# Optimization experiments

Hardware: AMD Instinct MI355X
Metric: run time of the kernel (lower is better)

Reference implementation:

```python
import jax, jax.numpy as jnp
import numpy as np

DK, DV, DMODEL, HEADNUM = 64, 64, 1024, 16
SEQ = 4096


def setup_inputs() -> dict:
    key = jax.random.key(0)
    ks = jax.random.split(key, 7)
    s = 0.02
    return {
        "q": jax.random.normal(ks[0], (SEQ, DMODEL), dtype=jnp.float32),
        "k": jax.random.normal(ks[1], (SEQ, DMODEL), dtype=jnp.float32),
        "v": jax.random.normal(ks[2], (SEQ, DMODEL), dtype=jnp.float32),
        # per-head projection weights, stored batched: [H, dmodel, dk]
        "Wq": jax.random.normal(ks[3], (HEADNUM, DMODEL, DK), dtype=jnp.float32) * s,
        "Wk": jax.random.normal(ks[4], (HEADNUM, DMODEL, DK), dtype=jnp.float32) * s,
        "Wv": jax.random.normal(ks[5], (HEADNUM, DMODEL, DV), dtype=jnp.float32) * s,
        # output linear (torch Linear weight [out, in]; y = x @ W.T)
        "Wo": jax.random.normal(ks[6], (DK * HEADNUM, DK * HEADNUM), dtype=jnp.float32) * s,
    }


def reference(q, k, v, Wq, Wk, Wv, Wo):
    # batched per-head projections: [H, S, dk/dv]
    qh = jnp.einsum("sd,hdk->hsk", q, Wq)
    kh = jnp.einsum("sd,hdk->hsk", k, Wk)
    vh = jnp.einsum("sd,hdv->hsv", v, Wv)
    scale = 1.0 / jnp.sqrt(jnp.asarray(DK, dtype=qh.dtype))
    scores = jnp.einsum("hqk,hsk->hqs", qh, kh) * scale  # [H, S, S]
    attn = jax.nn.softmax(scores, axis=-1)
    heads = jnp.einsum("hqs,hsv->hqv", attn, vh)  # [H, S, dv]
    # concat heads along feature dim: [S, H*dv]
    head_cat = jnp.transpose(heads, (1, 0, 2)).reshape(SEQ, HEADNUM * DV)
    return head_cat @ Wo.T
```

## Files before the change

### kernel.cpp

```cpp
#include <hip/hip_runtime.h>

#define SEQ 4096
#define DMODEL 1024
#define HEADNUM 16
#define DHEAD 64

typedef __attribute__((ext_vector_type(8))) short short8;
typedef __attribute__((ext_vector_type(4))) float f32x4;
typedef __attribute__((ext_vector_type(2))) float f32x2;
typedef __attribute__((ext_vector_type(16))) float f32x16;
typedef __attribute__((ext_vector_type(4))) int i32x4;

__device__ __forceinline__ short f2bf(float f) {
    unsigned u = __float_as_uint(f);
    u = (u + 0x7fffu + ((u >> 16) & 1u)) >> 16;
    return (short)u;
}

__device__ __forceinline__ float bf2f(short s) {
    return __uint_as_float(((unsigned)(unsigned short)s) << 16);
}

__device__ __forceinline__ short8 cvt8(const float4 a, const float4 b) {
    short8 r;
    r[0] = f2bf(a.x); r[1] = f2bf(a.y); r[2] = f2bf(a.z); r[3] = f2bf(a.w);
    r[4] = f2bf(b.x); r[5] = f2bf(b.y); r[6] = f2bf(b.z); r[7] = f2bf(b.w);
    return r;
}

__device__ __forceinline__ int cvtpk_bf16(float lo, float hi) {
    int r;
    asm("v_cvt_pk_bf16_f32 %0, %1, %2" : "=v"(r) : "v"(lo), "v"(hi));
    return r;
}

__device__ __forceinline__ float fexp2(float x) {
    float r;
    asm("v_exp_f32 %0, %1" : "=v"(r) : "v"(x));
    return r;
}

__device__ __forceinline__ void perml32(int& a, int& b) {
    asm("v_permlane32_swap_b32 %0, %1" : "+v"(a), "+v"(b));
}

__device__ __forceinline__ void gld16(const void* g, void* l) {
    __builtin_amdgcn_global_load_lds(
        (const __attribute__((address_space(1))) void*)g,
        (__attribute__((address_space(3))) void*)l, 16, 0, 0);
}

__global__ __launch_bounds__(256) void wtrans_kernel(
    const float* __restrict__ Wq, const float* __restrict__ Wk,
    const float* __restrict__ Wv, short* __restrict__ WT) {
    int which = blockIdx.z;
    const float* W = which == 0 ? Wq : (which == 1 ? Wk : Wv);
    short* dst = WT + (size_t)which * (HEADNUM * DHEAD * DMODEL);
    int h = blockIdx.y, d0 = blockIdx.x * 64;
    int tid = threadIdx.x;
    int c = tid & 63, r4 = tid >> 6;
    __shared__ short tl[64][66];
#pragma unroll
    for (int i = 0; i < 16; ++i) {
        int d = i * 4 + r4;
        tl[c][d] = f2bf(W[((size_t)h * DMODEL + d0 + d) * DHEAD + c]);
    }
    __syncthreads();
#pragma unroll
    for (int i = 0; i < 16; ++i) {
        int n = i * 4 + r4;
        dst[((size_t)h * DHEAD + n) * DMODEL + d0 + c] = tl[n][c];
    }
}

__global__ __launch_bounds__(256) void cast3_kernel(
    const float* __restrict__ q, const float* __restrict__ k,
    const float* __restrict__ v, short* __restrict__ qb,
    short* __restrict__ kb, short* __restrict__ vb) {
    int i = blockIdx.x * 256 + threadIdx.x;
    int seg = i >> 19;
    int off = i & ((1 << 19) - 1);
    const float* src = seg == 0 ? q : (seg == 1 ? k : v);
    short* dst = seg == 0 ? qb : (seg == 1 ? kb : vb);
    const float4* p = (const float4*)(src + (size_t)off * 8);
    *(short8*)(dst + (size_t)off * 8) = cvt8(p[0], p[1]);
}

__global__ __launch_bounds__(256) void cast_bf16_kernel(const float* __restrict__ in,
                                                        short* __restrict__ out, int n8) {
    int i = blockIdx.x * 256 + threadIdx.x;
    if (i >= n8) return;
    const float4* p = (const float4*)(in + (size_t)i * 8);
    *(short8*)(out + (size_t)i * 8) = cvt8(p[0], p[1]);
}

__global__ __launch_bounds__(256) void gemm_kernel(
    const short* __restrict__ A, const short* __restrict__ Bw,
    short* __restrict__ outb, float* __restrict__ outf, int mode) {
    int b = blockIdx.x;
    int wgid = (b & 7) * 64 + (b >> 3);
    int bi = wgid >> 3;
    int ni = wgid & 7;
    int i0 = bi * 64, j0 = ni * 128;

    int tid = threadIdx.x;
    int lane = tid & 63;
    int wv = tid >> 6;
    int l15 = lane & 15;
    int g = lane >> 4;
    int wm = wv >> 1, wn = wv & 1;

    __shared__ char glds[2][24576];

    int ja0 = tid * 16, ja1 = ja0 + 4096;
    int sa0 = (ja0 >> 7) * 2048 + ((ja0 & 127) ^ (((ja0 >> 7) & 7) << 4));
    int sa1 = (ja1 >> 7) * 2048 + ((ja1 & 127) ^ (((ja1 >> 7) & 7) << 4));
    int jb0 = tid * 16, jb1 = jb0 + 4096, jb2 = jb0 + 8192, jb3 = jb0 + 12288;
    int sb0 = (jb0 >> 7) * 2048 + ((jb0 & 127) ^ (((jb0 >> 7) & 7) << 4));
    int sb1 = (jb1 >> 7) * 2048 + ((jb1 & 127) ^ (((jb1 >> 7) & 7) << 4));
    int sb2 = (jb2 >> 7) * 2048 + ((jb2 & 127) ^ (((jb2 >> 7) & 7) << 4));
    int sb3 = (jb3 >> 7) * 2048 + ((jb3 & 127) ^ (((jb3 >> 7) & 7) << 4));

    const char* Ab = (const char*)A + (size_t)i0 * 2048;
    const char* Bb = (const char*)Bw + (size_t)j0 * 2048;

#define GSTAGE(bi_, kt_)                        \
    {                                           \
        char* la_ = glds[bi_];                  \
        char* lb_ = glds[bi_] + 8192;           \
        const char* As = Ab + (kt_) * 128;      \
        const char* Bs = Bb + (kt_) * 128;      \
        gld16(As + sa0, la_ + ja0);             \
        gld16(As + sa1, la_ + ja1);             \
        gld16(Bs + sb0, lb_ + jb0);             \
        gld16(Bs + sb1, lb_ + jb1);             \
        gld16(Bs + sb2, lb_ + jb2);             \
        gld16(Bs + sb3, lb_ + jb3);             \
    }

    f32x4 acc[2][4];
#pragma unroll
    for (int mm = 0; mm < 2; ++mm)
#pragma unroll
        for (int nn = 0; nn < 4; ++nn) acc[mm][nn] = (f32x4){0.f, 0.f, 0.f, 0.f};

    GSTAGE(0, 0);
    int cur = 0;
    for (int kt = 0; kt < 16; ++kt) {
        __syncthreads();
        if (kt < 15) GSTAGE(cur ^ 1, kt + 1);
        const char* la = glds[cur];
        const char* lb = glds[cur] + 8192;
#pragma unroll
        for (int kc = 0; kc < 2; ++kc) {
            short8 af[2], bf4[4];
#pragma unroll
            for (int mm = 0; mm < 2; ++mm) {
                int ra = wm * 32 + mm * 16 + l15;
                af[mm] = *(const short8*)(la + ra * 128 + ((kc * 64 + g * 16) ^ ((ra & 7) << 4)));
            }
#pragma unroll
            for (int nn = 0; nn < 4; ++nn) {
                int rb = wn * 64 + nn * 16 + l15;
                bf4[nn] = *(const short8*)(lb + rb * 128 + ((kc * 64 + g * 16) ^ ((rb & 7) << 4)));
            }
#pragma unroll
            for (int mm = 0; mm < 2; ++mm)
#pragma unroll
                for (int nn = 0; nn < 4; ++nn)
                    acc[mm][nn] = __builtin_amdgcn_mfma_f32_16x16x32_bf16(af[mm], bf4[nn], acc[mm][nn], 0, 0, 0);
        }
        cur ^= 1;
    }
#undef GSTAGE

#pragma unroll
    for (int mm = 0; mm < 2; ++mm)
#pragma unroll
        for (int nn = 0; nn < 4; ++nn)
#pragma unroll
            for (int r = 0; r < 4; ++r) {
                int mg = i0 + wm * 32 + mm * 16 + 4 * g + r;
                int ng = j0 + wn * 64 + nn * 16 + l15;
                float val = acc[mm][nn][r];
                if (mode == 0)      outb[(size_t)mg * 1024 + ng] = f2bf(val);
                else if (mode == 1) outb[(size_t)ng * 4096 + mg] = f2bf(val);
                else                outf[(size_t)mg * 1024 + ng] = val;
            }
}

__global__ __launch_bounds__(256, 4) void attn_kernel(
    const short* __restrict__ qh, const short* __restrict__ kh,
    const short* __restrict__ vt, short* __restrict__ po, float* __restrict__ ml) {
    int b = blockIdx.x;
    int wg = ((b & 7) << 7) | (b >> 3);
    int h = wg >> 6;
    int rem = wg & 63;
    int half = rem >> 5;
    int qb = rem & 31;

    int tid = threadIdx.x;
    int lane = tid & 63;
    int wv = tid >> 6;
    int l31 = lane & 31;
    int hh = lane >> 5;
    int qbase = qb * 128 + wv * 32;
    int kv0 = half * 2048;

    __shared__ __align__(16) char lds_all[3 * 8192];

    const short* qp = qh + (size_t)(qbase + l31) * 1024 + h * 64 + hh * 8;
    short8 bq0 = *(const short8*)(qp);
    short8 bq1 = *(const short8*)(qp + 16);
    short8 bq2 = *(const short8*)(qp + 32);
    short8 bq3 = *(const short8*)(qp + 48);

    const char* kbaseh = (const char*)kh + h * 128;
    const char* vbaseh = (const char*)vt + (size_t)h * 64 * 8192;

    int krow = tid >> 3;
    int kcol = (tid & 7) * 16;
    int ksrc = krow * 2048 + (kcol ^ ((krow & 7) << 4));
    int vrow = tid >> 2;
    int vswc = ((tid & 3) * 16) ^ (((vrow >> 1) & 3) << 4);
    size_t vsrcb = (size_t)vrow * 8192 + vswc;
    int ldst = tid * 16;

#define STAGE(P, kvg) {                                            \
    gld16(kbaseh + (size_t)(kvg) * 2048 + ksrc, (P) + ldst);       \
    gld16(vbaseh + (size_t)(kvg) * 2 + vsrcb, (P) + 4096 + ldst); }

    float mreg = 4.f, lsum = 0.f;
    f32x16 oa0 = {}, oa1 = {};

    int ksw = (l31 & 7) << 4;
    int hh16 = hh * 16;
    int vswz = (l31 >> 1) & 3;
    const float C1 = 0.18033688f;
    const float L2E = 1.44269504f;

    char* p0 = lds_all;
    char* p1 = lds_all + 8192;
    char* p2 = lds_all + 16384;

    STAGE(p0, kv0);
    STAGE(p1, kv0 + 32);

#define VMW(n) asm volatile("s_waitcnt vmcnt(" #n ")" ::: "memory")

#define COMPUTE(KP) {                                                          \
    const char* kp_ = (KP);                                                    \
    const char* vp_ = (KP) + 4096;                                             \
    short8 ak0 = *(const short8*)(kp_ + l31 * 128 + ((0   + hh16) ^ ksw));     \
    short8 ak1 = *(const short8*)(kp_ + l31 * 128 + ((32  + hh16) ^ ksw));     \
    short8 ak2 = *(const short8*)(kp_ + l31 * 128 + ((64  + hh16) ^ ksw));     \
    short8 ak3 = *(const short8*)(kp_ + l31 * 128 + ((96  + hh16) ^ ksw));     \
    f32x16 s_ = {};                                                            \
    s_ = __builtin_amdgcn_mfma_f32_32x32x16_bf16(ak0, bq0, s_, 0, 0, 0);       \
    s_ = __builtin_amdgcn_mfma_f32_32x32x16_bf16(ak1, bq1, s_, 0, 0, 0);       \
    s_ = __builtin_amdgcn_mfma_f32_32x32x16_bf16(ak2, bq2, s_, 0, 0, 0);       \
    s_ = __builtin_amdgcn_mfma_f32_32x32x16_bf16(ak3, bq3, s_, 0, 0, 0);       \
    float x0 = fmaxf(fmaxf(s_[0], s_[1]), fmaxf(s_[2], s_[3]));                \
    float x1 = fmaxf(fmaxf(s_[4], s_[5]), fmaxf(s_[6], s_[7]));                \
    float x2 = fmaxf(fmaxf(s_[8], s_[9]), fmaxf(s_[10], s_[11]));              \
    float x3 = fmaxf(fmaxf(s_[12], s_[13]), fmaxf(s_[14], s_[15]));            \
    float pm = fmaxf(fmaxf(x0, x1), fmaxf(x2, x3)) * 0.125f;                   \
    if (__any(pm > mreg + 8.f)) {                                              \
        float pmq = fmaxf(pm, __shfl_xor(pm, 32));                             \
        float nm = fmaxf(mreg, pmq);                                           \
        float al = fexp2((mreg - nm) * L2E);                                   \
        mreg = nm; lsum *= al;                                                 \
        _Pragma("unroll")                                                      \
        for (int i_ = 0; i_ < 16; ++i_) { oa0[i_] *= al; oa1[i_] *= al; }      \
    }                                                                          \
    float mL = mreg * L2E;                                                     \
    float e_[16];                                                              \
    _Pragma("unroll")                                                          \
    for (int i_ = 0; i_ < 16; ++i_) e_[i_] = fexp2(fmaf(s_[i_], C1, -mL));     \
    lsum += ((e_[0]+e_[1])+(e_[2]+e_[3])) + ((e_[4]+e_[5])+(e_[6]+e_[7]))      \
          + ((e_[8]+e_[9])+(e_[10]+e_[11])) + ((e_[12]+e_[13])+(e_[14]+e_[15])); \
    int pk0 = cvtpk_bf16(e_[0], e_[1]),   pk1 = cvtpk_bf16(e_[2], e_[3]);      \
    int pk2 = cvtpk_bf16(e_[4], e_[5]),   pk3 = cvtpk_bf16(e_[6], e_[7]);      \
    int pk4 = cvtpk_bf16(e_[8], e_[9]),   pk5 = cvtpk_bf16(e_[10], e_[11]);    \
    int pk6 = cvtpk_bf16(e_[12], e_[13]), pk7 = cvtpk_bf16(e_[14], e_[15]);    \
    perml32(pk0, pk2); perml32(pk1, pk3);                                      \
    perml32(pk4, pk6); perml32(pk5, pk7);                                      \
    i32x4 pc0v; pc0v[0] = pk0; pc0v[1] = pk1; pc0v[2] = pk2; pc0v[3] = pk3;    \
    i32x4 pc1v; pc1v[0] = pk4; pc1v[1] = pk5; pc1v[2] = pk6; pc1v[3] = pk7;    \
    short8 pc0 = *(short8*)&pc0v;                                              \
    short8 pc1 = *(short8*)&pc1v;                                              \
    short8 av00 = *(const short8*)(vp_ + l31 * 64 + (((0 + hh) ^ vswz) << 4)); \
    short8 av01 = *(const short8*)(vp_ + l31 * 64 + (((2 + hh) ^ vswz) << 4)); \
    short8 av10 = *(const short8*)(vp_ + (32 + l31) * 64 + (((0 + hh) ^ vswz) << 4)); \
    short8 av11 = *(const short8*)(vp_ + (32 + l31) * 64 + (((2 + hh) ^ vswz) << 4)); \
    oa0 = __builtin_amdgcn_mfma_f32_32x32x16_bf16(av00, pc0, oa0, 0, 0, 0);    \
    oa0 = __builtin_amdgcn_mfma_f32_32x32x16_bf16(av01, pc1, oa0, 0, 0, 0);    \
    oa1 = __builtin_amdgcn_mfma_f32_32x32x16_bf16(av10, pc0, oa1, 0, 0, 0);    \
    oa1 = __builtin_amdgcn_mfma_f32_32x32x16_bf16(av11, pc1, oa1, 0, 0, 0); }

    for (int t = 0; t < 62; ++t) {
        VMW(2);
        __builtin_amdgcn_s_barrier();
        STAGE(p2, kv0 + (t + 2) * 32);
        COMPUTE(p0);
        char* tp = p0; p0 = p1; p1 = p2; p2 = tp;
    }
    VMW(2);
    __builtin_amdgcn_s_barrier();
    COMPUTE(p0);
    { char* tp = p0; p0 = p1; p1 = p2; p2 = tp; }
    VMW(0);
    __builtin_amdgcn_s_barrier();
    COMPUTE(p0);
#undef COMPUTE
#undef STAGE
#undef VMW

    float lt = lsum + __shfl_xor(lsum, 32);
    int q = qbase + l31;
    if (hh == 0) {
        f32x2 mlv; mlv[0] = mreg; mlv[1] = lt;
        *(f32x2*)(ml + ((size_t)(half * 16 + h) * 4096 + q) * 2) = mlv;
    }
    short* pr = po + (size_t)(half * 4096 + q) * 1024 + h * 64 + hh * 4;
#pragma unroll
    for (int rp = 0; rp < 8; ++rp) {
        int dvb = ((2 * rp) & 3) + 8 * (rp >> 1);
        *(int*)(pr + dvb) = cvtpk_bf16(oa0[2 * rp], oa0[2 * rp + 1]);
        *(int*)(pr + 32 + dvb) = cvtpk_bf16(oa1[2 * rp], oa1[2 * rp + 1]);
    }
}

__global__ __launch_bounds__(256) void attn_reduce_kernel(
    const short* __restrict__ po, const float* __restrict__ ml,
    short* __restrict__ hc) {
    int idx = blockIdx.x * 256 + threadIdx.x;
    int q = idx >> 7;
    int cb = (idx & 127) * 8;
    int h = cb >> 6;
    f32x2 ml0 = *(const f32x2*)(ml + ((size_t)(h)*4096 + q) * 2);
    f32x2 ml1 = *(const f32x2*)(ml + ((size_t)(16 + h) * 4096 + q) * 2);
    float M = fmaxf(ml0[0], ml1[0]);
    float w0 = fexp2((ml0[0] - M) * 1.44269504f);
    float w1 = fexp2((ml1[0] - M) * 1.44269504f);
    float inv = 1.f / (ml0[1] * w0 + ml1[1] * w1);
    w0 *= inv; w1 *= inv;
    short8 p0 = *(const short8*)(po + (size_t)q * 1024 + cb);
    short8 p1 = *(const short8*)(po + (size_t)(4096 + q) * 1024 + cb);
    short8 r;
#pragma unroll
    for (int j = 0; j < 8; ++j)
        r[j] = f2bf(bf2f(p0[j]) * w0 + bf2f(p1[j]) * w1);
    *(short8*)(hc + (size_t)q * 1024 + cb) = r;
}

extern "C" void kernel_launch(void* const* d_in, const int* in_sizes, int n_in,
                              void* d_out, int out_size, void* d_ws, size_t ws_size,
                              hipStream_t stream) {
    const float* q  = (const float*)d_in[0];
    const float* k  = (const float*)d_in[1];
    const float* v  = (const float*)d_in[2];
    const float* Wq = (const float*)d_in[3];
    const float* Wk = (const float*)d_in[4];
    const float* Wv = (const float*)d_in[5];
    const float* Wo = (const float*)d_in[6];
    float* out = (float*)d_out;

    char* ws = (char*)d_ws;
    const size_t MB = 1u << 20;
    short* WqT  = (short*)(ws + 0 * MB);
    short* WkT  = (short*)(ws + 2 * MB);
    short* WvT  = (short*)(ws + 4 * MB);
    short* qh   = (short*)(ws + 6 * MB);
    short* kh   = (short*)(ws + 14 * MB);
    short* vt   = (short*)(ws + 22 * MB);
    short* hcqb = (short*)(ws + 30 * MB);
    float* mlbuf = (float*)(ws + 38 * MB);
    short* Wob  = WqT;
    short* kb = (short*)d_out;
    short* vb = (short*)d_out + SEQ * DMODEL;
    short* po = (short*)d_out;

    wtrans_kernel<<<dim3(DMODEL / 64, HEADNUM, 3), 256, 0, stream>>>(Wq, Wk, Wv, WqT);

    cast3_kernel<<<dim3(3 * SEQ * DMODEL / 8 / 256), 256, 0, stream>>>(
        q, k, v, hcqb, kb, vb);

    gemm_kernel<<<dim3(512), 256, 0, stream>>>(hcqb, WqT, qh, 0, 0);
    gemm_kernel<<<dim3(512), 256, 0, stream>>>(kb, WkT, kh, 0, 0);
    gemm_kernel<<<dim3(512), 256, 0, stream>>>(vb, WvT, vt, 0, 1);

    int n8w = DMODEL * DMODEL / 8;
    cast_bf16_kernel<<<dim3(n8w / 256), 256, 0, stream>>>(Wo, Wob, n8w);

    attn_kernel<<<dim3(1024), 256, 0, stream>>>(qh, kh, vt, po, mlbuf);

    attn_reduce_kernel<<<dim3(2048), 256, 0, stream>>>(po, mlbuf, hcqb);

    gemm_kernel<<<dim3(512), 256, 0, stream>>>(hcqb, Wob, 0, out, 2);
}
```

Baseline: 189.8 us.

## Process two query tiles per wave in attention and triple-buffer GEMM loads

```diff
diff --git a/kernel.cpp b/kernel.cpp
--- a/kernel.cpp
+++ b/kernel.cpp
@@ -110,7 +110,7 @@
     int g = lane >> 4;
     int wm = wv >> 1, wn = wv & 1;
 
-    __shared__ char glds[2][24576];
+    __shared__ __align__(16) char glds[3 * 24576];
 
     int ja0 = tid * 16, ja1 = ja0 + 4096;
     int sa0 = (ja0 >> 7) * 2048 + ((ja0 & 127) ^ (((ja0 >> 7) & 7) << 4));
@@ -124,10 +124,10 @@
     const char* Ab = (const char*)A + (size_t)i0 * 2048;
     const char* Bb = (const char*)Bw + (size_t)j0 * 2048;
 
-#define GSTAGE(bi_, kt_)                        \
+#define GSTAGE(P, kt_)                          \
     {                                           \
-        char* la_ = glds[bi_];                  \
-        char* lb_ = glds[bi_] + 8192;           \
+        char* la_ = (P);                        \
+        char* lb_ = (P) + 8192;                 \
         const char* As = Ab + (kt_) * 128;      \
         const char* Bs = Bb + (kt_) * 128;      \
         gld16(As + sa0, la_ + ja0);             \
@@ -144,35 +144,55 @@
 #pragma unroll
         for (int nn = 0; nn < 4; ++nn) acc[mm][nn] = (f32x4){0.f, 0.f, 0.f, 0.f};
 
-    GSTAGE(0, 0);
-    int cur = 0;
-    for (int kt = 0; kt < 16; ++kt) {
-        __syncthreads();
-        if (kt < 15) GSTAGE(cur ^ 1, kt + 1);
-        const char* la = glds[cur];
-        const char* lb = glds[cur] + 8192;
-#pragma unroll
-        for (int kc = 0; kc < 2; ++kc) {
-            short8 af[2], bf4[4];
-#pragma unroll
-            for (int mm = 0; mm < 2; ++mm) {
-                int ra = wm * 32 + mm * 16 + l15;
-                af[mm] = *(const short8*)(la + ra * 128 + ((kc * 64 + g * 16) ^ ((ra & 7) << 4)));
-            }
-#pragma unroll
-            for (int nn = 0; nn < 4; ++nn) {
-                int rb = wn * 64 + nn * 16 + l15;
-                bf4[nn] = *(const short8*)(lb + rb * 128 + ((kc * 64 + g * 16) ^ ((rb & 7) << 4)));
-            }
-#pragma unroll
-            for (int mm = 0; mm < 2; ++mm)
-#pragma unroll
-                for (int nn = 0; nn < 4; ++nn)
-                    acc[mm][nn] = __builtin_amdgcn_mfma_f32_16x16x32_bf16(af[mm], bf4[nn], acc[mm][nn], 0, 0, 0);
-        }
-        cur ^= 1;
-    }
+#define GCOMPUTE(P)                                                                           \
+    {                                                                                         \
+        const char* la = (P);                                                                 \
+        const char* lb = (P) + 8192;                                                          \
+        _Pragma("unroll")                                                                     \
+        for (int kc = 0; kc < 2; ++kc) {                                                      \
+            short8 af[2], bf4[4];                                                             \
+            _Pragma("unroll")                                                                 \
+            for (int mm = 0; mm < 2; ++mm) {                                                  \
+                int ra = wm * 32 + mm * 16 + l15;                                             \
+                af[mm] = *(const short8*)(la + ra * 128 + ((kc * 64 + g * 16) ^ ((ra & 7) << 4))); \
+            }                                                                                 \
+            _Pragma("unroll")                                                                 \
+            for (int nn = 0; nn < 4; ++nn) {                                                  \
+                int rb = wn * 64 + nn * 16 + l15;                                             \
+                bf4[nn] = *(const short8*)(lb + rb * 128 + ((kc * 64 + g * 16) ^ ((rb & 7) << 4))); \
+            }                                                                                 \
+            _Pragma("unroll")                                                                 \
+            for (int mm = 0; mm < 2; ++mm)                                                    \
+                _Pragma("unroll")                                                             \
+                for (int nn = 0; nn < 4; ++nn)                                                \
+                    acc[mm][nn] = __builtin_amdgcn_mfma_f32_16x16x32_bf16(af[mm], bf4[nn], acc[mm][nn], 0, 0, 0); \
+        }                                                                                     \
+    }
+
+#define VMW(n) asm volatile("s_waitcnt vmcnt(" #n ")" ::: "memory")
+
+    char* P0 = glds;
+    char* P1 = glds + 24576;
+    char* P2 = glds + 49152;
+    GSTAGE(P0, 0);
+    GSTAGE(P1, 1);
+    for (int kt = 0; kt < 14; ++kt) {
+        VMW(6);
+        __builtin_amdgcn_s_barrier();
+        GSTAGE(P2, kt + 2);
+        GCOMPUTE(P0);
+        char* tp = P0; P0 = P1; P1 = P2; P2 = tp;
+    }
+    VMW(6);
+    __builtin_amdgcn_s_barrier();
+    GCOMPUTE(P0);
+    { char* tp = P0; P0 = P1; P1 = P2; P2 = tp; }
+    VMW(0);
+    __builtin_amdgcn_s_barrier();
+    GCOMPUTE(P0);
 #undef GSTAGE
+#undef GCOMPUTE
+#undef VMW
 
 #pragma unroll
     for (int mm = 0; mm < 2; ++mm)
@@ -189,31 +209,36 @@
             }
 }
 
-__global__ __launch_bounds__(256, 4) void attn_kernel(
+__global__ __launch_bounds__(256, 2) void attn_kernel(
     const short* __restrict__ qh, const short* __restrict__ kh,
     const short* __restrict__ vt, short* __restrict__ po, float* __restrict__ ml) {
     int b = blockIdx.x;
-    int wg = ((b & 7) << 7) | (b >> 3);
-    int h = wg >> 6;
-    int rem = wg & 63;
-    int half = rem >> 5;
-    int qb = rem & 31;
+    int wg = ((b & 7) << 6) | (b >> 3);
+    int h = wg >> 5;
+    int rem = wg & 31;
+    int half = rem >> 4;
+    int qb = rem & 15;
 
     int tid = threadIdx.x;
     int lane = tid & 63;
     int wv = tid >> 6;
     int l31 = lane & 31;
     int hh = lane >> 5;
-    int qbase = qb * 128 + wv * 32;
+    int qbase = qb * 256 + wv * 64;
     int kv0 = half * 2048;
 
     __shared__ __align__(16) char lds_all[3 * 8192];
 
-    const short* qp = qh + (size_t)(qbase + l31) * 1024 + h * 64 + hh * 8;
-    short8 bq0 = *(const short8*)(qp);
-    short8 bq1 = *(const short8*)(qp + 16);
-    short8 bq2 = *(const short8*)(qp + 32);
-    short8 bq3 = *(const short8*)(qp + 48);
+    const short* qpA = qh + (size_t)(qbase + l31) * 1024 + h * 64 + hh * 8;
+    const short* qpB = qpA + 32 * 1024;
+    short8 bqA0 = *(const short8*)(qpA);
+    short8 bqA1 = *(const short8*)(qpA + 16);
+    short8 bqA2 = *(const short8*)(qpA + 32);
+    short8 bqA3 = *(const short8*)(qpA + 48);
+    short8 bqB0 = *(const short8*)(qpB);
+    short8 bqB1 = *(const short8*)(qpB + 16);
+    short8 bqB2 = *(const short8*)(qpB + 32);
+    short8 bqB3 = *(const short8*)(qpB + 48);
 
     const char* kbaseh = (const char*)kh + h * 128;
     const char* vbaseh = (const char*)vt + (size_t)h * 64 * 8192;
@@ -230,8 +255,8 @@
     gld16(kbaseh + (size_t)(kvg) * 2048 + ksrc, (P) + ldst);       \
     gld16(vbaseh + (size_t)(kvg) * 2 + vsrcb, (P) + 4096 + ldst); }
 
-    float mreg = 4.f, lsum = 0.f;
-    f32x16 oa0 = {}, oa1 = {};
+    float mregA = 4.f, lsumA = 0.f, mregB = 4.f, lsumB = 0.f;
+    f32x16 oaA0 = {}, oaA1 = {}, oaB0 = {}, oaB1 = {};
 
     int ksw = (l31 & 7) << 4;
     int hh16 = hh * 16;
@@ -247,6 +272,29 @@
     STAGE(p1, kv0 + 32);
 
 #define VMW(n) asm volatile("s_waitcnt vmcnt(" #n ")" ::: "memory")
+
+#define SOFTMAX(S, MREG, LSUM, PC0, PC1) {                                     \
+    float mL = (MREG) * L2E;                                                   \
+    float e_[16];                                                              \
+    _Pragma("unroll")                                                          \
+    for (int i_ = 0; i_ < 16; ++i_) e_[i_] = fexp2(fmaf((S)[i_], C1, -mL));    \
+    LSUM += ((e_[0]+e_[1])+(e_[2]+e_[3])) + ((e_[4]+e_[5])+(e_[6]+e_[7]))      \
+          + ((e_[8]+e_[9])+(e_[10]+e_[11])) + ((e_[12]+e_[13])+(e_[14]+e_[15])); \
+    int pk0 = cvtpk_bf16(e_[0], e_[1]),   pk1 = cvtpk_bf16(e_[2], e_[3]);      \
+    int pk2 = cvtpk_bf16(e_[4], e_[5]),   pk3 = cvtpk_bf16(e_[6], e_[7]);      \
+    int pk4 = cvtpk_bf16(e_[8], e_[9]),   pk5 = cvtpk_bf16(e_[10], e_[11]);    \
+    int pk6 = cvtpk_bf16(e_[12], e_[13]), pk7 = cvtpk_bf16(e_[14], e_[15]);    \
+    perml32(pk0, pk2); perml32(pk1, pk3);                                      \
+    perml32(pk4, pk6); perml32(pk5, pk7);                                      \
+    i32x4 v0_; v0_[0] = pk0; v0_[1] = pk1; v0_[2] = pk2; v0_[3] = pk3;         \
+    i32x4 v1_; v1_[0] = pk4; v1_[1] = pk5; v1_[2] = pk6; v1_[3] = pk7;         \
+    PC0 = *(short8*)&v0_;                                                      \
+    PC1 = *(short8*)&v1_; }
+
+#define MAX16(S) fmaxf(fmaxf(fmaxf(fmaxf((S)[0],(S)[1]),fmaxf((S)[2],(S)[3])),   \
+                             fmaxf(fmaxf((S)[4],(S)[5]),fmaxf((S)[6],(S)[7]))),  \
+                       fmaxf(fmaxf(fmaxf((S)[8],(S)[9]),fmaxf((S)[10],(S)[11])), \
+                             fmaxf(fmaxf((S)[12],(S)[13]),fmaxf((S)[14],(S)[15]))))
 
 #define COMPUTE(KP) {                                                          \
     const char* kp_ = (KP);                                                    \
@@ -255,48 +303,51 @@
     short8 ak1 = *(const short8*)(kp_ + l31 * 128 + ((32  + hh16) ^ ksw));     \
     short8 ak2 = *(const short8*)(kp_ + l31 * 128 + ((64  + hh16) ^ ksw));     \
     short8 ak3 = *(const short8*)(kp_ + l31 * 128 + ((96  + hh16) ^ ksw));     \
-    f32x16 s_ = {};                                                            \
-    s_ = __builtin_amdgcn_mfma_f32_32x32x16_bf16(ak0, bq0, s_, 0, 0, 0);       \
-    s_ = __builtin_amdgcn_mfma_f32_32x32x16_bf16(ak1, bq1, s_, 0, 0, 0);       \
-    s_ = __builtin_amdgcn_mfma_f32_32x32x16_bf16(ak2, bq2, s_, 0, 0, 0);       \
-    s_ = __builtin_amdgcn_mfma_f32_32x32x16_bf16(ak3, bq3, s_, 0, 0, 0);       \
-    float x0 = fmaxf(fmaxf(s_[0], s_[1]), fmaxf(s_[2], s_[3]));                \
-    float x1 = fmaxf(fmaxf(s_[4], s_[5]), fmaxf(s_[6], s_[7]));                \
-    float x2 = fmaxf(fmaxf(s_[8], s_[9]), fmaxf(s_[10], s_[11]));              \
-    float x3 = fmaxf(fmaxf(s_[12], s_[13]), fmaxf(s_[14], s_[15]));            \
-    float pm = fmaxf(fmaxf(x0, x1), fmaxf(x2, x3)) * 0.125f;                   \
-    if (__any(pm > mreg + 8.f)) {                                              \
-        float pmq = fmaxf(pm, __shfl_xor(pm, 32));                             \
-        float nm = fmaxf(mreg, pmq);                                           \
-        float al = fexp2((mreg - nm) * L2E);                                   \
-        mreg = nm; lsum *= al;                                                 \
+    f32x16 sA = {}, sB = {};                                                   \
+    __builtin_amdgcn_s_setprio(1);                                             \
+    sA = __builtin_amdgcn_mfma_f32_32x32x16_bf16(ak0, bqA0, sA, 0, 0, 0);      \
+    sA = __builtin_amdgcn_mfma_f32_32x32x16_bf16(ak1, bqA1, sA, 0, 0, 0);      \
+    sA = __builtin_amdgcn_mfma_f32_32x32x16_bf16(ak2, bqA2, sA, 0, 0, 0);      \
+    sA = __builtin_amdgcn_mfma_f32_32x32x16_bf16(ak3, bqA3, sA, 0, 0, 0);      \
+    sB = __builtin_amdgcn_mfma_f32_32x32x16_bf16(ak0, bqB0, sB, 0, 0, 0);      \
+    sB = __builtin_amdgcn_mfma_f32_32x32x16_bf16(ak1, bqB1, sB, 0, 0, 0);      \
+    sB = __builtin_amdgcn_mfma_f32_32x32x16_bf16(ak2, bqB2, sB, 0, 0, 0);      \
+    sB = __builtin_amdgcn_mfma_f32_32x32x16_bf16(ak3, bqB3, sB, 0, 0, 0);      \
+    __builtin_amdgcn_s_setprio(0);                                             \
+    float pmA = MAX16(sA) * 0.125f;                                            \
+    float pmB = MAX16(sB) * 0.125f;                                            \
+    if (__any(fmaxf(pmA - mregA, pmB - mregB) > 8.f)) {                        \
+        float pqA = fmaxf(pmA, __shfl_xor(pmA, 32));                           \
+        float nmA = fmaxf(mregA, pqA);                                         \
+        float alA = fexp2((mregA - nmA) * L2E);                                \
+        mregA = nmA; lsumA *= alA;                                             \
+        float pqB = fmaxf(pmB, __shfl_xor(pmB, 32));                           \
+        float nmB = fmaxf(mregB, pqB);                                         \
+        float alB = fexp2((mregB - nmB) * L2E);                                \
+        mregB = nmB; lsumB *= alB;                                             \
         _Pragma("unroll")                                                      \
-        for (int i_ = 0; i_ < 16; ++i_) { oa0[i_] *= al; oa1[i_] *= al; }      \
+        for (int i_ = 0; i_ < 16; ++i_) {                                      \
+            oaA0[i_] *= alA; oaA1[i_] *= alA;                                  \
+            oaB0[i_] *= alB; oaB1[i_] *= alB;                                  \
+        }                                                                      \
     }                                                                          \
-    float mL = mreg * L2E;                                                     \
-    float e_[16];                                                              \
-    _Pragma("unroll")                                                          \
-    for (int i_ = 0; i_ < 16; ++i_) e_[i_] = fexp2(fmaf(s_[i_], C1, -mL));     \
-    lsum += ((e_[0]+e_[1])+(e_[2]+e_[3])) + ((e_[4]+e_[5])+(e_[6]+e_[7]))      \
-          + ((e_[8]+e_[9])+(e_[10]+e_[11])) + ((e_[12]+e_[13])+(e_[14]+e_[15])); \
-    int pk0 = cvtpk_bf16(e_[0], e_[1]),   pk1 = cvtpk_bf16(e_[2], e_[3]);      \
-    int pk2 = cvtpk_bf16(e_[4], e_[5]),   pk3 = cvtpk_bf16(e_[6], e_[7]);      \
-    int pk4 = cvtpk_bf16(e_[8], e_[9]),   pk5 = cvtpk_bf16(e_[10], e_[11]);    \
-    int pk6 = cvtpk_bf16(e_[12], e_[13]), pk7 = cvtpk_bf16(e_[14], e_[15]);    \
-    perml32(pk0, pk2); perml32(pk1, pk3);                                      \
-    perml32(pk4, pk6); perml32(pk5, pk7);                                      \
-    i32x4 pc0v; pc0v[0] = pk0; pc0v[1] = pk1; pc0v[2] = pk2; pc0v[3] = pk3;    \
-    i32x4 pc1v; pc1v[0] = pk4; pc1v[1] = pk5; pc1v[2] = pk6; pc1v[3] = pk7;    \
-    short8 pc0 = *(short8*)&pc0v;                                              \
-    short8 pc1 = *(short8*)&pc1v;                                              \
+    short8 pcA0, pcA1, pcB0, pcB1;                                             \
+    SOFTMAX(sA, mregA, lsumA, pcA0, pcA1);                                     \
+    SOFTMAX(sB, mregB, lsumB, pcB0, pcB1);                                     \
     short8 av00 = *(const short8*)(vp_ + l31 * 64 + (((0 + hh) ^ vswz) << 4)); \
     short8 av01 = *(const short8*)(vp_ + l31 * 64 + (((2 + hh) ^ vswz) << 4)); \
     short8 av10 = *(const short8*)(vp_ + (32 + l31) * 64 + (((0 + hh) ^ vswz) << 4)); \
     short8 av11 = *(const short8*)(vp_ + (32 + l31) * 64 + (((2 + hh) ^ vswz) << 4)); \
-    oa0 = __builtin_amdgcn_mfma_f32_32x32x16_bf16(av00, pc0, oa0, 0, 0, 0);    \
-    oa0 = __builtin_amdgcn_mfma_f32_32x32x16_bf16(av01, pc1, oa0, 0, 0, 0);    \
-    oa1 = __builtin_amdgcn_mfma_f32_32x32x16_bf16(av10, pc0, oa1, 0, 0, 0);    \
-    oa1 = __builtin_amdgcn_mfma_f32_32x32x16_bf16(av11, pc1, oa1, 0, 0, 0); }
+    __builtin_amdgcn_s_setprio(1);                                             \
+    oaA0 = __builtin_amdgcn_mfma_f32_32x32x16_bf16(av00, pcA0, oaA0, 0, 0, 0); \
+    oaA0 = __builtin_amdgcn_mfma_f32_32x32x16_bf16(av01, pcA1, oaA0, 0, 0, 0); \
+    oaA1 = __builtin_amdgcn_mfma_f32_32x32x16_bf16(av10, pcA0, oaA1, 0, 0, 0); \
+    oaA1 = __builtin_amdgcn_mfma_f32_32x32x16_bf16(av11, pcA1, oaA1, 0, 0, 0); \
+    oaB0 = __builtin_amdgcn_mfma_f32_32x32x16_bf16(av00, pcB0, oaB0, 0, 0, 0); \
+    oaB0 = __builtin_amdgcn_mfma_f32_32x32x16_bf16(av01, pcB1, oaB0, 0, 0, 0); \
+    oaB1 = __builtin_amdgcn_mfma_f32_32x32x16_bf16(av10, pcB0, oaB1, 0, 0, 0); \
+    oaB1 = __builtin_amdgcn_mfma_f32_32x32x16_bf16(av11, pcB1, oaB1, 0, 0, 0); \
+    __builtin_amdgcn_s_setprio(0); }
 
     for (int t = 0; t < 62; ++t) {
         VMW(2);
@@ -313,21 +364,40 @@
     __builtin_amdgcn_s_barrier();
     COMPUTE(p0);
 #undef COMPUTE
+#undef SOFTMAX
+#undef MAX16
 #undef STAGE
 #undef VMW
 
-    float lt = lsum + __shfl_xor(lsum, 32);
-    int q = qbase + l31;
-    if (hh == 0) {
-        f32x2 mlv; mlv[0] = mreg; mlv[1] = lt;
-        *(f32x2*)(ml + ((size_t)(half * 16 + h) * 4096 + q) * 2) = mlv;
-    }
-    short* pr = po + (size_t)(half * 4096 + q) * 1024 + h * 64 + hh * 4;
-#pragma unroll
-    for (int rp = 0; rp < 8; ++rp) {
-        int dvb = ((2 * rp) & 3) + 8 * (rp >> 1);
-        *(int*)(pr + dvb) = cvtpk_bf16(oa0[2 * rp], oa0[2 * rp + 1]);
-        *(int*)(pr + 32 + dvb) = cvtpk_bf16(oa1[2 * rp], oa1[2 * rp + 1]);
+    {
+        float ltA = lsumA + __shfl_xor(lsumA, 32);
+        int qA = qbase + l31;
+        if (hh == 0) {
+            f32x2 mlv; mlv[0] = mregA; mlv[1] = ltA;
+            *(f32x2*)(ml + ((size_t)(half * 16 + h) * 4096 + qA) * 2) = mlv;
+        }
+        short* pr = po + (size_t)(half * 4096 + qA) * 1024 + h * 64 + hh * 4;
+#pragma unroll
+        for (int rp = 0; rp < 8; ++rp) {
+            int dvb = ((2 * rp) & 3) + 8 * (rp >> 1);
+            *(int*)(pr + dvb) = cvtpk_bf16(oaA0[2 * rp], oaA0[2 * rp + 1]);
+            *(int*)(pr + 32 + dvb) = cvtpk_bf16(oaA1[2 * rp], oaA1[2 * rp + 1]);
+        }
+    }
+    {
+        float ltB = lsumB + __shfl_xor(lsumB, 32);
+        int qB = qbase + 32 + l31;
+        if (hh == 0) {
+            f32x2 mlv; mlv[0] = mregB; mlv[1] = ltB;
+            *(f32x2*)(ml + ((size_t)(half * 16 + h) * 4096 + qB) * 2) = mlv;
+        }
+        short* pr = po + (size_t)(half * 4096 + qB) * 1024 + h * 64 + hh * 4;
+#pragma unroll
+        for (int rp = 0; rp < 8; ++rp) {
+            int dvb = ((2 * rp) & 3) + 8 * (rp >> 1);
+            *(int*)(pr + dvb) = cvtpk_bf16(oaB0[2 * rp], oaB0[2 * rp + 1]);
+            *(int*)(pr + 32 + dvb) = cvtpk_bf16(oaB1[2 * rp], oaB1[2 * rp + 1]);
+        }
     }
 }
 
@@ -393,7 +463,7 @@
     int n8w = DMODEL * DMODEL / 8;
     cast_bf16_kernel<<<dim3(n8w / 256), 256, 0, stream>>>(Wo, Wob, n8w);
 
-    attn_kernel<<<dim3(1024), 256, 0, stream>>>(qh, kh, vt, po, mlbuf);
+    attn_kernel<<<dim3(512), 256, 0, stream>>>(qh, kh, vt, po, mlbuf);
 
     attn_reduce_kernel<<<dim3(2048), 256, 0, stream>>>(po, mlbuf, hcqb);
 
```

Result: no change. 189.8 us (-0.0%).
